# Kernel tuning notes

Hardware: AMD Instinct MI355X
Metric: run time of the kernel (lower is better)

## Reference

```python
import jax, jax.numpy as jnp
import numpy as np


def setup_inputs() -> dict:
    key = jax.random.key(0)
    k1, k2 = jax.random.split(key)
    B, S_ENC, S_DEC, D = 8, 2048, 2048, 512
    enc_outputs = jax.random.normal(k1, (B, S_ENC, D), dtype=jnp.float32)
    dec_outputs = jax.random.normal(k2, (B, S_DEC, D), dtype=jnp.float32)
    return {"enc_outputs": enc_outputs, "dec_outputs": dec_outputs}


def reference(enc_outputs, dec_outputs):
    # scores: [B, S_dec, S_enc] = dec @ enc^T  (no scaling, no mask — matches original)
    s_t = jnp.einsum('bqd,bkd->bqk', dec_outputs, enc_outputs)
    a_t = jax.nn.softmax(s_t, axis=-1)
    # context: [B, S_dec, D]
    c_t = jnp.einsum('bqk,bkd->bqd', a_t, enc_outputs)
    return c_t
```

## Files before the change

kernel.cpp:

```cpp
#include <hip/hip_runtime.h>
#include <cstdint>
#include <cstddef>

#define Bb 8
#define Ss 2048
#define Dd 512

typedef _Float16 half8 __attribute__((ext_vector_type(8)));
typedef _Float16 half4_ __attribute__((ext_vector_type(4)));
typedef _Float16 half2_t __attribute__((ext_vector_type(2)));
typedef float f32x4 __attribute__((ext_vector_type(4)));

static __device__ __forceinline__ void gload_lds16(const void* g, void* l) {
  __builtin_amdgcn_global_load_lds((const __attribute__((address_space(1))) void*)g,
                                   (__attribute__((address_space(3))) void*)l,
                                   16, 0, 0);
}

__global__ void k0_prep(const float* __restrict__ enc, const float* __restrict__ dec,
                        _Float16* __restrict__ enc16, _Float16* __restrict__ encT,
                        _Float16* __restrict__ dec16) {
  __shared__ _Float16 tb[8][64][8];
  int bid = blockIdx.x;
  int b = bid & 7, kt = (bid >> 3) & 31, dt = bid >> 8;
  int key0 = kt * 64, d0 = dt * 64;
  int t = threadIdx.x;

  {
    size_t off = (size_t)bid * 4096 + (size_t)t * 16;
    const float4* p = (const float4*)(dec + off);
    float4 a0 = p[0], a1 = p[1], a2 = p[2], a3 = p[3];
    half8 h0, h1;
    h0[0] = (_Float16)a0.x; h0[1] = (_Float16)a0.y; h0[2] = (_Float16)a0.z; h0[3] = (_Float16)a0.w;
    h0[4] = (_Float16)a1.x; h0[5] = (_Float16)a1.y; h0[6] = (_Float16)a1.z; h0[7] = (_Float16)a1.w;
    h1[0] = (_Float16)a2.x; h1[1] = (_Float16)a2.y; h1[2] = (_Float16)a2.z; h1[3] = (_Float16)a2.w;
    h1[4] = (_Float16)a3.x; h1[5] = (_Float16)a3.y; h1[6] = (_Float16)a3.z; h1[7] = (_Float16)a3.w;
    *(half8*)(dec16 + off) = h0;
    *(half8*)(dec16 + off + 8) = h1;
  }

  const float* src = enc + ((size_t)b * Ss + key0) * Dd + d0;
  _Float16* d16 = enc16 + ((size_t)b * Ss + key0) * Dd + d0;
#pragma unroll
  for (int p = 0; p < 4; ++p) {
    int row = p * 16 + (t >> 4);
    int c = (t & 15) * 4;
    float4 a = *(const float4*)(src + (size_t)row * Dd + c);
    half4_ h;
    h[0] = (_Float16)a.x; h[1] = (_Float16)a.y; h[2] = (_Float16)a.z; h[3] = (_Float16)a.w;
    *(half4_*)(d16 + (size_t)row * Dd + c) = h;
    int K = row >> 3, k = row & 7;
#pragma unroll
    for (int i = 0; i < 4; ++i) tb[K][c + i][k] = h[i];
  }
  __syncthreads();

  _Float16* oT = encT + ((size_t)b * Dd + d0) * Ss + key0;
#pragma unroll
  for (int q = 0; q < 2; ++q) {
    int d = q * 32 + (t >> 3);
    int k8 = (t & 7) * 8;
    half8 v = *(const half8*)&tb[k8 >> 3][d][0];
    *(half8*)(oT + (size_t)d * Ss + k8) = v;
  }
}

__launch_bounds__(256, 2)
__global__ void k1_qk(const _Float16* __restrict__ A, const _Float16* __restrict__ Bm,
                      _Float16* __restrict__ S, half2_t* __restrict__ pms) {
  __shared__ __align__(16) _Float16 lA[128 * 64];
  __shared__ __align__(16) _Float16 lB[128 * 64];
  int bid = blockIdx.x;
  int b = bid & 7;
  int t = bid >> 3;
  int tm = t & 15, tn = t >> 4;
  int tid = threadIdx.x;
  int w = tid >> 6, L = tid & 63;
  int wm = w & 1, wn = w >> 1;

  const _Float16* Ag = A + ((size_t)b * Ss + (size_t)tm * 128) * Dd;
  const _Float16* Bg = Bm + ((size_t)b * Ss + (size_t)tn * 128) * Dd;

  int rowS[4], colS[4], ldsOff[4];
#pragma unroll
  for (int i = 0; i < 4; ++i) {
    int se = (w * 4 + i) * 512 + L * 8;
    int row = se >> 6;
    int blk = (se >> 3) & 7;
    rowS[i] = row;
    colS[i] = (blk ^ (row & 7)) << 3;
    ldsOff[i] = se;
  }

  f32x4 acc[4][4];
#pragma unroll
  for (int mt = 0; mt < 4; ++mt)
#pragma unroll
    for (int nt = 0; nt < 4; ++nt) acc[mt][nt] = (f32x4){0.f, 0.f, 0.f, 0.f};

  int g = L >> 4, lm = L & 15;

  for (int k0 = 0; k0 < Dd; k0 += 64) {
    __syncthreads();
#pragma unroll
    for (int i = 0; i < 4; ++i) {
      gload_lds16(Ag + (size_t)rowS[i] * Dd + k0 + colS[i], lA + ldsOff[i]);
      gload_lds16(Bg + (size_t)rowS[i] * Dd + k0 + colS[i], lB + ldsOff[i]);
    }
    __syncthreads();
#pragma unroll
    for (int ds = 0; ds < 64; ds += 32) {
      half8 af[4], bf[4];
#pragma unroll
      for (int mt = 0; mt < 4; ++mt) {
        int row = wm * 64 + mt * 16 + lm;
        int blk = ((ds >> 3) + g) ^ (row & 7);
        af[mt] = *(const half8*)(lA + row * 64 + blk * 8);
      }
#pragma unroll
      for (int nt = 0; nt < 4; ++nt) {
        int row = wn * 64 + nt * 16 + lm;
        int blk = ((ds >> 3) + g) ^ (row & 7);
        bf[nt] = *(const half8*)(lB + row * 64 + blk * 8);
      }
#pragma unroll
      for (int mt = 0; mt < 4; ++mt)
#pragma unroll
        for (int nt = 0; nt < 4; ++nt)
          acc[mt][nt] = __builtin_amdgcn_mfma_f32_16x16x32_f16(af[mt], bf[nt], acc[mt][nt], 0, 0, 0);
    }
  }

  size_t rowbase = (size_t)b * Ss;
#pragma unroll
  for (int mt = 0; mt < 4; ++mt) {
#pragma unroll
    for (int r = 0; r < 4; ++r) {
      int row_g = tm * 128 + wm * 64 + mt * 16 + g * 4 + r;
      _Float16* Srow = S + (rowbase + row_g) * Ss + (size_t)tn * 128 + wn * 64 + lm;
      float rm = -1e30f;
#pragma unroll
      for (int nt = 0; nt < 4; ++nt) rm = fmaxf(rm, acc[mt][nt][r]);
      rm = fmaxf(rm, __shfl_xor(rm, 1));
      rm = fmaxf(rm, __shfl_xor(rm, 2));
      rm = fmaxf(rm, __shfl_xor(rm, 4));
      rm = fmaxf(rm, __shfl_xor(rm, 8));
      _Float16 mh = (_Float16)rm;
      float mf = (float)mh;
      float sum = 0.f;
#pragma unroll
      for (int nt = 0; nt < 4; ++nt) {
        float e = __expf(acc[mt][nt][r] - mf);
        Srow[nt * 16] = (_Float16)e;
        sum += e;
      }
      sum += __shfl_xor(sum, 1);
      sum += __shfl_xor(sum, 2);
      sum += __shfl_xor(sum, 4);
      sum += __shfl_xor(sum, 8);
      if (lm == 0) {
        half2_t st; st.x = mh; st.y = (_Float16)sum;
        pms[(rowbase + row_g) * 32 + tn * 2 + wn] = st;
      }
    }
  }
}

__launch_bounds__(256, 4)
__global__ void k3_pv(const _Float16* __restrict__ P, const _Float16* __restrict__ Vt,
                      const half2_t* __restrict__ pms, float* __restrict__ C) {
  __shared__ __align__(16) _Float16 lA[128 * 64];
  __shared__ __align__(16) _Float16 lB[64 * 64];
  __shared__ float fctL[32 * 128];
  int bid = blockIdx.x;
  int b = bid & 7;
  int t = bid >> 3;
  int tm = t & 15, tn = t >> 4;
  int tid = threadIdx.x;
  int w = tid >> 6, L = tid & 63;
  int wm = w & 1, wn = w >> 1;

  if (tid < 128) {
    const half2_t* pr = pms + ((size_t)b * Ss + (size_t)tm * 128 + tid) * 32;
    float mc[32], sc[32];
#pragma unroll
    for (int c = 0; c < 32; ++c) { half2_t v = pr[c]; mc[c] = (float)v.x; sc[c] = (float)v.y; }
    float m = mc[0];
#pragma unroll
    for (int c = 1; c < 32; ++c) m = fmaxf(m, mc[c]);
    float tot = 0.f;
    float ef[32];
#pragma unroll
    for (int c = 0; c < 32; ++c) { ef[c] = __expf(mc[c] - m); tot += sc[c] * ef[c]; }
    float rinv = 1.0f / tot;
#pragma unroll
    for (int c = 0; c < 32; ++c) fctL[c * 128 + tid] = ef[c] * rinv;
  }

  const _Float16* Ag = P + ((size_t)b * Ss + (size_t)tm * 128) * Ss;
  const _Float16* Bg = Vt + ((size_t)b * Dd + (size_t)tn * 64) * Ss;

  int rowA[4], colA[4], offA[4];
#pragma unroll
  for (int i = 0; i < 4; ++i) {
    int se = (w * 4 + i) * 512 + L * 8;
    int row = se >> 6;
    int blk = (se >> 3) & 7;
    rowA[i] = row;
    colA[i] = (blk ^ (row & 7)) << 3;
    offA[i] = se;
  }
  int rowB[2], colB[2], offB[2];
#pragma unroll
  for (int i = 0; i < 2; ++i) {
    int se = (w * 2 + i) * 512 + L * 8;
    int row = se >> 6;
    int blk = (se >> 3) & 7;
    rowB[i] = row;
    colB[i] = (blk ^ (row & 7)) << 3;
    offB[i] = se;
  }

  f32x4 acc[4][2];
#pragma unroll
  for (int mt = 0; mt < 4; ++mt)
#pragma unroll
    for (int nt = 0; nt < 2; ++nt) acc[mt][nt] = (f32x4){0.f, 0.f, 0.f, 0.f};

  int g = L >> 4, lm = L & 15;

  for (int k0 = 0; k0 < Ss; k0 += 64) {
    __syncthreads();
#pragma unroll
    for (int i = 0; i < 4; ++i)
      gload_lds16(Ag + (size_t)rowA[i] * Ss + k0 + colA[i], lA + offA[i]);
#pragma unroll
    for (int i = 0; i < 2; ++i)
      gload_lds16(Bg + (size_t)rowB[i] * Ss + k0 + colB[i], lB + offB[i]);
    __syncthreads();
    _Float16 fh[4];
#pragma unroll
    for (int mt = 0; mt < 4; ++mt)
      fh[mt] = (_Float16)fctL[(k0 >> 6) * 128 + wm * 64 + mt * 16 + lm];
#pragma unroll
    for (int ds = 0; ds < 64; ds += 32) {
      half8 af[4], bf[2];
#pragma unroll
      for (int mt = 0; mt < 4; ++mt) {
        int row = wm * 64 + mt * 16 + lm;
        int blk = ((ds >> 3) + g) ^ (row & 7);
        af[mt] = *(const half8*)(lA + row * 64 + blk * 8);
#pragma unroll
        for (int j = 0; j < 8; ++j) af[mt][j] *= fh[mt];
      }
#pragma unroll
      for (int nt = 0; nt < 2; ++nt) {
        int row = wn * 32 + nt * 16 + lm;
        int blk = ((ds >> 3) + g) ^ (row & 7);
        bf[nt] = *(const half8*)(lB + row * 64 + blk * 8);
      }
#pragma unroll
      for (int mt = 0; mt < 4; ++mt)
#pragma unroll
        for (int nt = 0; nt < 2; ++nt)
          acc[mt][nt] = __builtin_amdgcn_mfma_f32_16x16x32_f16(af[mt], bf[nt], acc[mt][nt], 0, 0, 0);
    }
  }

#pragma unroll
  for (int mt = 0; mt < 4; ++mt) {
#pragma unroll
    for (int r = 0; r < 4; ++r) {
      int row_g = tm * 128 + wm * 64 + mt * 16 + g * 4 + r;
      float* Crow = C + ((size_t)b * Ss + row_g) * Dd + (size_t)tn * 64 + wn * 32 + lm;
#pragma unroll
      for (int nt = 0; nt < 2; ++nt) Crow[nt * 16] = acc[mt][nt][r];
    }
  }
}

extern "C" void kernel_launch(void* const* d_in, const int* in_sizes, int n_in,
                              void* d_out, int out_size, void* d_ws, size_t ws_size,
                              hipStream_t stream) {
  const float* enc = (const float*)d_in[0];
  const float* dec = (const float*)d_in[1];
  float* out = (float*)d_out;

  const size_t nElem = (size_t)Bb * Ss * Dd;
  const size_t nS = (size_t)Bb * Ss * Ss;

  _Float16* dec16 = (_Float16*)d_ws;
  _Float16* enc16 = dec16 + nElem;
  _Float16* encT = enc16 + nElem;
  _Float16* Sp = encT + nElem;
  half2_t* pms = (half2_t*)(Sp + nS);

  size_t need = nElem * 2 * 3 + nS * 2 + (size_t)Bb * Ss * 32 * 4;
  if (ws_size < need) return;

  k0_prep<<<2048, 256, 0, stream>>>(enc, dec, enc16, encT, dec16);
  k1_qk<<<2048, 256, 0, stream>>>(dec16, enc16, Sp, pms);
  k3_pv<<<1024, 256, 0, stream>>>(Sp, encT, pms, out);
}
```

Before: 206.0 us.

## Rewrite QK kernel with 256x256 tiles, 8 waves, double-buffered LDS pipeline

Replaces the 128x128-tile QK^T+partial-softmax kernel with a 256x256-tile, 512-thread version that uses 128KB of dynamic LDS. Global-to-LDS loads for the next K-slice are double-buffered and staggered across quarter-tile MFMA phases, with explicit vmcnt waits, barriers and setprio. The aim is more operand reuse per loaded byte and better overlap of loads with MFMA work. The old kernel is kept as a fallback for when the large shared-memory allocation is unavailable. In exchange it needs high register pressure and runs only 512 blocks.

```diff
diff --git a/kernel.cpp b/kernel.cpp
--- a/kernel.cpp
+++ b/kernel.cpp
@@ -65,9 +65,191 @@
   }
 }
 
-__launch_bounds__(256, 2)
+template<int QM, int QN>
+static __device__ __forceinline__ void mfma16(f32x4 (&acc)[8][4],
+                                              const half8 (&af)[4][2],
+                                              const half8 (&bf)[2][2]) {
+#pragma unroll
+  for (int ks = 0; ks < 2; ++ks)
+#pragma unroll
+    for (int mt2 = 0; mt2 < 4; ++mt2)
+#pragma unroll
+      for (int ntl = 0; ntl < 2; ++ntl)
+        acc[QM * 4 + mt2][QN * 2 + ntl] = __builtin_amdgcn_mfma_f32_16x16x32_f16(
+            af[mt2][ks], bf[ntl][ks], acc[QM * 4 + mt2][QN * 2 + ntl], 0, 0, 0);
+}
+
+#define WAITVM4 do { asm volatile("s_waitcnt vmcnt(4)" ::: "memory"); __builtin_amdgcn_sched_barrier(0); } while (0)
+#define WAITVM0 do { asm volatile("s_waitcnt vmcnt(0)" ::: "memory"); __builtin_amdgcn_sched_barrier(0); } while (0)
+#define BAR() __builtin_amdgcn_s_barrier()
+
+__launch_bounds__(512, 2)
 __global__ void k1_qk(const _Float16* __restrict__ A, const _Float16* __restrict__ Bm,
                       _Float16* __restrict__ S, half2_t* __restrict__ pms) {
+  extern __shared__ _Float16 smem[];
+  int bid = blockIdx.x;
+  int b = bid & 7;
+  int tt = bid >> 3;
+  int tm = tt & 7, tn = tt >> 3;
+  int tid = threadIdx.x;
+  int w = tid >> 6, L = tid & 63;
+  int wm = w >> 2, wn = w & 3;
+  int g = L >> 4, lm = L & 15;
+
+  const _Float16* Ag = A + ((size_t)b * Ss + (size_t)tm * 256) * Dd;
+  const _Float16* Bg = Bm + ((size_t)b * Ss + (size_t)tn * 256) * Dd;
+
+  int sl0 = (w * 2 + 0) * 512 + L * 8;
+  int sl1 = (w * 2 + 1) * 512 + L * 8;
+  const _Float16* gA[2][2];
+  const _Float16* gB[2][2];
+#pragma unroll
+  for (int j = 0; j < 2; ++j) {
+    int sl = j ? sl1 : sl0;
+    int lr = sl >> 6;
+    int oct = (sl >> 3) & 7;
+#pragma unroll
+    for (int ga = 0; ga < 2; ++ga) {
+      int row = (lr >> 6) * 128 + ga * 64 + (lr & 63);
+      gA[ga][j] = Ag + (size_t)row * Dd + ((oct ^ (row & 7)) * 8);
+    }
+#pragma unroll
+    for (int qn = 0; qn < 2; ++qn) {
+      int row = (lr >> 5) * 64 + qn * 32 + (lr & 31);
+      gB[qn][j] = Bg + (size_t)row * Dd + ((oct ^ (row & 7)) * 8);
+    }
+  }
+
+  f32x4 acc[8][4];
+#pragma unroll
+  for (int i = 0; i < 8; ++i)
+#pragma unroll
+    for (int j = 0; j < 4; ++j) acc[i][j] = (f32x4){0.f, 0.f, 0.f, 0.f};
+
+  int o80 = ((0 * 4 + g) ^ (lm & 7)) * 8;
+  int o81 = ((1 * 4 + g) ^ (lm & 7)) * 8;
+  int aBase = (wm * 64 + lm) * 64;
+  int bBase = (wn * 32 + lm) * 64;
+
+  gload_lds16(gA[0][0], smem + sl0);
+  gload_lds16(gA[0][1], smem + sl1);
+  gload_lds16(gB[0][0], smem + 32768 + sl0);
+  gload_lds16(gB[0][1], smem + 32768 + sl1);
+  gload_lds16(gB[1][0], smem + 32768 + 8192 + sl0);
+  gload_lds16(gB[1][1], smem + 32768 + 8192 + sl1);
+  gload_lds16(gA[1][0], smem + 8192 + sl0);
+  gload_lds16(gA[1][1], smem + 8192 + sl1);
+  WAITVM4;
+  BAR();
+
+  const int NT = Dd / 64;
+#pragma unroll 2
+  for (int t = 0; t < NT; ++t) {
+    int cb = t & 1, nb = cb ^ 1;
+    const _Float16* pAr = smem + cb * 16384 + aBase;
+    const _Float16* pBr = smem + 32768 + cb * 16384 + bBase;
+    _Float16* lAn = smem + nb * 16384;
+    _Float16* lBn = smem + 32768 + nb * 16384;
+    int k0n = (t + 1) * 64;
+    bool pre = (t < NT - 1);
+    half8 af[4][2], bf[2][2];
+
+#pragma unroll
+    for (int mt2 = 0; mt2 < 4; ++mt2) {
+      af[mt2][0] = *(const half8*)(pAr + mt2 * 1024 + o80);
+      af[mt2][1] = *(const half8*)(pAr + mt2 * 1024 + o81);
+    }
+#pragma unroll
+    for (int ntl = 0; ntl < 2; ++ntl) {
+      bf[ntl][0] = *(const half8*)(pBr + ntl * 1024 + o80);
+      bf[ntl][1] = *(const half8*)(pBr + ntl * 1024 + o81);
+    }
+    if (pre) { gload_lds16(gA[0][0] + k0n, lAn + sl0); gload_lds16(gA[0][1] + k0n, lAn + sl1); }
+    BAR();
+    __builtin_amdgcn_s_setprio(1);
+    mfma16<0, 0>(acc, af, bf);
+    __builtin_amdgcn_s_setprio(0);
+    if (pre) WAITVM4;
+    BAR();
+
+#pragma unroll
+    for (int ntl = 0; ntl < 2; ++ntl) {
+      bf[ntl][0] = *(const half8*)(pBr + 8192 + ntl * 1024 + o80);
+      bf[ntl][1] = *(const half8*)(pBr + 8192 + ntl * 1024 + o81);
+    }
+    if (pre) { gload_lds16(gB[0][0] + k0n, lBn + sl0); gload_lds16(gB[0][1] + k0n, lBn + sl1); }
+    BAR();
+    __builtin_amdgcn_s_setprio(1);
+    mfma16<0, 1>(acc, af, bf);
+    __builtin_amdgcn_s_setprio(0);
+    if (pre) WAITVM4;
+    BAR();
+
+#pragma unroll
+    for (int mt2 = 0; mt2 < 4; ++mt2) {
+      af[mt2][0] = *(const half8*)(pAr + 8192 + mt2 * 1024 + o80);
+      af[mt2][1] = *(const half8*)(pAr + 8192 + mt2 * 1024 + o81);
+    }
+    if (pre) { gload_lds16(gB[1][0] + k0n, lBn + 8192 + sl0); gload_lds16(gB[1][1] + k0n, lBn + 8192 + sl1); }
+    BAR();
+    __builtin_amdgcn_s_setprio(1);
+    mfma16<1, 1>(acc, af, bf);
+    __builtin_amdgcn_s_setprio(0);
+    BAR();
+
+#pragma unroll
+    for (int ntl = 0; ntl < 2; ++ntl) {
+      bf[ntl][0] = *(const half8*)(pBr + ntl * 1024 + o80);
+      bf[ntl][1] = *(const half8*)(pBr + ntl * 1024 + o81);
+    }
+    if (pre) { gload_lds16(gA[1][0] + k0n, lAn + 8192 + sl0); gload_lds16(gA[1][1] + k0n, lAn + 8192 + sl1); }
+    BAR();
+    __builtin_amdgcn_s_setprio(1);
+    mfma16<1, 0>(acc, af, bf);
+    __builtin_amdgcn_s_setprio(0);
+    if (t < NT - 2) { WAITVM4; }
+    else if (t == NT - 2) { WAITVM0; }
+    BAR();
+  }
+
+  size_t rowbase = (size_t)b * Ss;
+#pragma unroll
+  for (int mt = 0; mt < 8; ++mt) {
+#pragma unroll
+    for (int r = 0; r < 4; ++r) {
+      int row_g = tm * 256 + wm * 128 + mt * 16 + g * 4 + r;
+      _Float16* Srow = S + (rowbase + row_g) * Ss + (size_t)tn * 256 + wn * 64 + lm;
+      float rm = -1e30f;
+#pragma unroll
+      for (int nt = 0; nt < 4; ++nt) rm = fmaxf(rm, acc[mt][nt][r]);
+      rm = fmaxf(rm, __shfl_xor(rm, 1));
+      rm = fmaxf(rm, __shfl_xor(rm, 2));
+      rm = fmaxf(rm, __shfl_xor(rm, 4));
+      rm = fmaxf(rm, __shfl_xor(rm, 8));
+      _Float16 mh = (_Float16)rm;
+      float mf = (float)mh;
+      float sum = 0.f;
+#pragma unroll
+      for (int nt = 0; nt < 4; ++nt) {
+        float e = __expf(acc[mt][nt][r] - mf);
+        Srow[nt * 16] = (_Float16)e;
+        sum += e;
+      }
+      sum += __shfl_xor(sum, 1);
+      sum += __shfl_xor(sum, 2);
+      sum += __shfl_xor(sum, 4);
+      sum += __shfl_xor(sum, 8);
+      if (lm == 0) {
+        half2_t st; st.x = mh; st.y = (_Float16)sum;
+        pms[(rowbase + row_g) * 32 + tn * 4 + wn] = st;
+      }
+    }
+  }
+}
+
+__launch_bounds__(256, 2)
+__global__ void k1_qk_fb(const _Float16* __restrict__ A, const _Float16* __restrict__ Bm,
+                         _Float16* __restrict__ S, half2_t* __restrict__ pms) {
   __shared__ __align__(16) _Float16 lA[128 * 64];
   __shared__ __align__(16) _Float16 lB[128 * 64];
   int bid = blockIdx.x;
@@ -298,7 +480,27 @@
   size_t need = nElem * 2 * 3 + nS * 2 + (size_t)Bb * Ss * 32 * 4;
   if (ws_size < need) return;
 
+  static int g_k1_big = -1;
+  if (g_k1_big < 0) {
+    int ok = 0;
+    (void)hipFuncSetAttribute(reinterpret_cast<const void*>(&k1_qk),
+                              hipFuncAttributeMaxDynamicSharedMemorySize, 131072);
+    hipFuncAttributes fa;
+    if (hipFuncGetAttributes(&fa, reinterpret_cast<const void*>(&k1_qk)) == hipSuccess &&
+        fa.maxDynamicSharedSizeBytes >= 131072) ok = 1;
+    if (!ok) {
+      int dev = 0, maxShm = 0;
+      (void)hipGetDevice(&dev);
+      if (hipDeviceGetAttribute(&maxShm, hipDeviceAttributeMaxSharedMemoryPerBlock, dev) ==
+              hipSuccess && maxShm >= 131072) ok = 1;
+    }
+    g_k1_big = ok;
+  }
+
   k0_prep<<<2048, 256, 0, stream>>>(enc, dec, enc16, encT, dec16);
-  k1_qk<<<2048, 256, 0, stream>>>(dec16, enc16, Sp, pms);
+  if (g_k1_big)
+    k1_qk<<<512, 512, 131072, stream>>>(dec16, enc16, Sp, pms);
+  else
+    k1_qk_fb<<<2048, 256, 0, stream>>>(dec16, enc16, Sp, pms);
   k3_pv<<<1024, 256, 0, stream>>>(Sp, encT, pms, out);
 }
```

After: 205.9 us. No clear change (-0.0%).

## Fuse QK, softmax and PV into single flash-attention kernel with online softmax

Applied to the files above, without the earlier changes.

Replaces the two-kernel path (QK scores written to a full fp16 S matrix in global memory, then a PV kernel rescaling by per-chunk max/sum) with one fused flash-style kernel. Each block owns 64 query rows, keeps Q fragments in registers, double-buffers 32-key E tiles in LDS via async loads, does an online softmax with conditional rescaling, and reads V directly from global into registers. This removes the large S round trip through HBM but launches only 256 blocks, uses many barriers per 32-key step, and has small per-iteration MFMA work, so occupancy and sync overhead may limit it.

```diff
diff --git a/kernel.cpp b/kernel.cpp
--- a/kernel.cpp
+++ b/kernel.cpp
@@ -8,7 +8,6 @@
 
 typedef _Float16 half8 __attribute__((ext_vector_type(8)));
 typedef _Float16 half4_ __attribute__((ext_vector_type(4)));
-typedef _Float16 half2_t __attribute__((ext_vector_type(2)));
 typedef float f32x4 __attribute__((ext_vector_type(4)));
 
 static __device__ __forceinline__ void gload_lds16(const void* g, void* l) {
@@ -65,32 +64,53 @@
   }
 }
 
-__launch_bounds__(256, 2)
-__global__ void k1_qk(const _Float16* __restrict__ A, const _Float16* __restrict__ Bm,
-                      _Float16* __restrict__ S, half2_t* __restrict__ pms) {
-  __shared__ __align__(16) _Float16 lA[128 * 64];
-  __shared__ __align__(16) _Float16 lB[128 * 64];
+#define WAITVM(N) do { asm volatile("s_waitcnt vmcnt(" #N ")" ::: "memory"); __builtin_amdgcn_sched_barrier(0); } while (0)
+#define LGKM0 asm volatile("s_waitcnt lgkmcnt(0)" ::: "memory")
+#define BARR() __builtin_amdgcn_s_barrier()
+
+__launch_bounds__(512, 2)
+__global__ void kf_attn(const _Float16* __restrict__ Qm, const _Float16* __restrict__ Em,
+                        const _Float16* __restrict__ Vt, float* __restrict__ C) {
+  extern __shared__ _Float16 smem[];
+  _Float16* pS = smem + 32768;
+  float* fb = (float*)(smem + 34816);
+  float* wMax = fb;
+  float* wSum = fb + 128;
+  float* fct  = fb + 256;
+  float* negm = fb + 320;
+  float* mst  = fb + 384;
+  float* lst  = fb + 448;
+  int*   flg  = (int*)(fb + 512);
+
   int bid = blockIdx.x;
-  int b = bid & 7;
-  int t = bid >> 3;
-  int tm = t & 15, tn = t >> 4;
+  int b = bid & 7, qt = bid >> 3;
+  int q0 = qt * 64;
   int tid = threadIdx.x;
   int w = tid >> 6, L = tid & 63;
-  int wm = w & 1, wn = w >> 1;
-
-  const _Float16* Ag = A + ((size_t)b * Ss + (size_t)tm * 128) * Dd;
-  const _Float16* Bg = Bm + ((size_t)b * Ss + (size_t)tn * 128) * Dd;
-
-  int rowS[4], colS[4], ldsOff[4];
-#pragma unroll
-  for (int i = 0; i < 4; ++i) {
-    int se = (w * 4 + i) * 512 + L * 8;
-    int row = se >> 6;
-    int blk = (se >> 3) & 7;
-    rowS[i] = row;
-    colS[i] = (blk ^ (row & 7)) << 3;
-    ldsOff[i] = se;
-  }
+  int g = L >> 4, lm = L & 15;
+  int wm4 = w >> 1, wn2 = w & 1;
+  int k7 = lm & 7;
+
+  half8 qf[16];
+  {
+    const _Float16* qp = Qm + ((size_t)(b * Ss + q0 + wm4 * 16 + lm)) * Dd + g * 8;
+#pragma unroll
+    for (int ks = 0; ks < 16; ++ks) qf[ks] = *(const half8*)(qp + ks * 32);
+  }
+
+  if (tid < 64) { mst[tid] = -1e30f; lst[tid] = 0.f; }
+
+  const _Float16* eg[4]; int els[4];
+#pragma unroll
+  for (int r = 0; r < 4; ++r) {
+    int key = r * 8 + w;
+    els[r] = key * 512 + L * 8;
+    eg[r] = Em + ((size_t)(b * Ss) + key) * Dd + ((L ^ (key & 7)) * 8);
+  }
+  uint64_t vb[4];
+#pragma unroll
+  for (int nt = 0; nt < 4; ++nt)
+    vb[nt] = (uint64_t)(uintptr_t)(Vt + ((size_t)(b * Dd + w * 64 + nt * 16 + lm)) * Ss + g * 8);
 
   f32x4 acc[4][4];
 #pragma unroll
@@ -98,185 +118,121 @@
 #pragma unroll
     for (int nt = 0; nt < 4; ++nt) acc[mt][nt] = (f32x4){0.f, 0.f, 0.f, 0.f};
 
-  int g = L >> 4, lm = L & 15;
-
-  for (int k0 = 0; k0 < Dd; k0 += 64) {
-    __syncthreads();
-#pragma unroll
-    for (int i = 0; i < 4; ++i) {
-      gload_lds16(Ag + (size_t)rowS[i] * Dd + k0 + colS[i], lA + ldsOff[i]);
-      gload_lds16(Bg + (size_t)rowS[i] * Dd + k0 + colS[i], lB + ldsOff[i]);
-    }
-    __syncthreads();
-#pragma unroll
-    for (int ds = 0; ds < 64; ds += 32) {
-      half8 af[4], bf[4];
-#pragma unroll
-      for (int mt = 0; mt < 4; ++mt) {
-        int row = wm * 64 + mt * 16 + lm;
-        int blk = ((ds >> 3) + g) ^ (row & 7);
-        af[mt] = *(const half8*)(lA + row * 64 + blk * 8);
-      }
-#pragma unroll
-      for (int nt = 0; nt < 4; ++nt) {
-        int row = wn * 64 + nt * 16 + lm;
-        int blk = ((ds >> 3) + g) ^ (row & 7);
-        bf[nt] = *(const half8*)(lB + row * 64 + blk * 8);
-      }
+#pragma unroll
+  for (int r = 0; r < 4; ++r) gload_lds16(eg[r], smem + els[r]);
+  LGKM0;
+  BARR();
+
+#pragma unroll 1
+  for (int t = 0; t < 64; ++t) {
+    bool pre = t < 63;
+    const _Float16* eC = smem + ((t & 1) << 14);
+    _Float16* eN = smem + (((t + 1) & 1) << 14);
+
+    f32x4 bfr[4];
+#pragma unroll
+    for (int nt = 0; nt < 4; ++nt) {
+      uint64_t a = vb[nt] + (uint64_t)t * 64;
+      asm volatile("global_load_dwordx4 %0, %1, off" : "=v"(bfr[nt]) : "v"(a));
+    }
+    if (pre) {
+#pragma unroll
+      for (int r = 0; r < 4; ++r) gload_lds16(eg[r] + (size_t)(t + 1) * 16384, eN + els[r]);
+    }
+    if (pre) { WAITVM(8); } else { WAITVM(4); }
+    BARR();
+
+    f32x4 s0 = (f32x4){0.f, 0.f, 0.f, 0.f}, s1 = (f32x4){0.f, 0.f, 0.f, 0.f};
+    const _Float16* eRow = eC + (wn2 * 16 + lm) * 512;
+    __builtin_amdgcn_s_setprio(1);
+#pragma unroll
+    for (int ks = 0; ks < 16; ks += 2) {
+      half8 b0 = *(const half8*)(eRow + (((ks * 4 + g) ^ k7) << 3));
+      half8 b1 = *(const half8*)(eRow + ((((ks + 1) * 4 + g) ^ k7) << 3));
+      s0 = __builtin_amdgcn_mfma_f32_16x16x32_f16(qf[ks], b0, s0, 0, 0, 0);
+      s1 = __builtin_amdgcn_mfma_f32_16x16x32_f16(qf[ks + 1], b1, s1, 0, 0, 0);
+    }
+    __builtin_amdgcn_s_setprio(0);
+    f32x4 sa = s0 + s1;
+
+#pragma unroll
+    for (int r = 0; r < 4; ++r) {
+      float m = sa[r];
+      m = fmaxf(m, __shfl_xor(m, 1));
+      m = fmaxf(m, __shfl_xor(m, 2));
+      m = fmaxf(m, __shfl_xor(m, 4));
+      m = fmaxf(m, __shfl_xor(m, 8));
+      if (lm == 0) wMax[wn2 * 64 + wm4 * 16 + g * 4 + r] = m;
+    }
+    LGKM0; BARR();
+
+    if (tid < 64) {
+      float tmax = fmaxf(wMax[tid], wMax[64 + tid]);
+      float mo = mst[tid];
+      float mn = fmaxf(mo, tmax);
+      fct[tid] = __expf(mo - mn);
+      negm[tid] = mn;
+      mst[tid] = mn;
+      unsigned long long bal = __ballot(tmax > mo);
+      if (tid == 0) *flg = (bal != 0ULL) ? 1 : 0;
+    }
+    LGKM0; BARR();
+
+    int cc = wn2 * 2 + (lm >> 3);
+#pragma unroll
+    for (int r = 0; r < 4; ++r) {
+      int R = wm4 * 16 + g * 4 + r;
+      float p = __expf(sa[r] - negm[R]);
+      pS[R * 32 + (((cc ^ r) << 3) | k7)] = (_Float16)p;
+      float s = p;
+      s += __shfl_xor(s, 1); s += __shfl_xor(s, 2);
+      s += __shfl_xor(s, 4); s += __shfl_xor(s, 8);
+      if (lm == 0) wSum[wn2 * 64 + R] = s;
+    }
+    LGKM0; BARR();
+
+    if (tid < 64) lst[tid] = lst[tid] * fct[tid] + wSum[tid] + wSum[64 + tid];
+
+    if (*flg) {
 #pragma unroll
       for (int mt = 0; mt < 4; ++mt)
 #pragma unroll
-        for (int nt = 0; nt < 4; ++nt)
-          acc[mt][nt] = __builtin_amdgcn_mfma_f32_16x16x32_f16(af[mt], bf[nt], acc[mt][nt], 0, 0, 0);
-    }
-  }
-
-  size_t rowbase = (size_t)b * Ss;
-#pragma unroll
-  for (int mt = 0; mt < 4; ++mt) {
-#pragma unroll
-    for (int r = 0; r < 4; ++r) {
-      int row_g = tm * 128 + wm * 64 + mt * 16 + g * 4 + r;
-      _Float16* Srow = S + (rowbase + row_g) * Ss + (size_t)tn * 128 + wn * 64 + lm;
-      float rm = -1e30f;
-#pragma unroll
-      for (int nt = 0; nt < 4; ++nt) rm = fmaxf(rm, acc[mt][nt][r]);
-      rm = fmaxf(rm, __shfl_xor(rm, 1));
-      rm = fmaxf(rm, __shfl_xor(rm, 2));
-      rm = fmaxf(rm, __shfl_xor(rm, 4));
-      rm = fmaxf(rm, __shfl_xor(rm, 8));
-      _Float16 mh = (_Float16)rm;
-      float mf = (float)mh;
-      float sum = 0.f;
-#pragma unroll
-      for (int nt = 0; nt < 4; ++nt) {
-        float e = __expf(acc[mt][nt][r] - mf);
-        Srow[nt * 16] = (_Float16)e;
-        sum += e;
-      }
-      sum += __shfl_xor(sum, 1);
-      sum += __shfl_xor(sum, 2);
-      sum += __shfl_xor(sum, 4);
-      sum += __shfl_xor(sum, 8);
-      if (lm == 0) {
-        half2_t st; st.x = mh; st.y = (_Float16)sum;
-        pms[(rowbase + row_g) * 32 + tn * 2 + wn] = st;
-      }
-    }
-  }
-}
-
-__launch_bounds__(256, 4)
-__global__ void k3_pv(const _Float16* __restrict__ P, const _Float16* __restrict__ Vt,
-                      const half2_t* __restrict__ pms, float* __restrict__ C) {
-  __shared__ __align__(16) _Float16 lA[128 * 64];
-  __shared__ __align__(16) _Float16 lB[64 * 64];
-  __shared__ float fctL[32 * 128];
-  int bid = blockIdx.x;
-  int b = bid & 7;
-  int t = bid >> 3;
-  int tm = t & 15, tn = t >> 4;
-  int tid = threadIdx.x;
-  int w = tid >> 6, L = tid & 63;
-  int wm = w & 1, wn = w >> 1;
-
-  if (tid < 128) {
-    const half2_t* pr = pms + ((size_t)b * Ss + (size_t)tm * 128 + tid) * 32;
-    float mc[32], sc[32];
-#pragma unroll
-    for (int c = 0; c < 32; ++c) { half2_t v = pr[c]; mc[c] = (float)v.x; sc[c] = (float)v.y; }
-    float m = mc[0];
-#pragma unroll
-    for (int c = 1; c < 32; ++c) m = fmaxf(m, mc[c]);
-    float tot = 0.f;
-    float ef[32];
-#pragma unroll
-    for (int c = 0; c < 32; ++c) { ef[c] = __expf(mc[c] - m); tot += sc[c] * ef[c]; }
-    float rinv = 1.0f / tot;
-#pragma unroll
-    for (int c = 0; c < 32; ++c) fctL[c * 128 + tid] = ef[c] * rinv;
-  }
-
-  const _Float16* Ag = P + ((size_t)b * Ss + (size_t)tm * 128) * Ss;
-  const _Float16* Bg = Vt + ((size_t)b * Dd + (size_t)tn * 64) * Ss;
-
-  int rowA[4], colA[4], offA[4];
-#pragma unroll
-  for (int i = 0; i < 4; ++i) {
-    int se = (w * 4 + i) * 512 + L * 8;
-    int row = se >> 6;
-    int blk = (se >> 3) & 7;
-    rowA[i] = row;
-    colA[i] = (blk ^ (row & 7)) << 3;
-    offA[i] = se;
-  }
-  int rowB[2], colB[2], offB[2];
-#pragma unroll
-  for (int i = 0; i < 2; ++i) {
-    int se = (w * 2 + i) * 512 + L * 8;
-    int row = se >> 6;
-    int blk = (se >> 3) & 7;
-    rowB[i] = row;
-    colB[i] = (blk ^ (row & 7)) << 3;
-    offB[i] = se;
-  }
-
-  f32x4 acc[4][2];
+        for (int rr = 0; rr < 4; ++rr) {
+          float f = fct[mt * 16 + g * 4 + rr];
+#pragma unroll
+          for (int nt = 0; nt < 4; ++nt) acc[mt][nt][rr] *= f;
+        }
+    }
+
+    if (pre) { WAITVM(4); } else { WAITVM(0); }
+
+    half8 af[4];
+#pragma unroll
+    for (int mt = 0; mt < 4; ++mt)
+      af[mt] = *(const half8*)(pS + (mt * 16 + lm) * 32 + ((g ^ (lm & 3)) << 3));
+    __builtin_amdgcn_s_setprio(1);
+#pragma unroll
+    for (int mt = 0; mt < 4; ++mt)
+#pragma unroll
+      for (int nt = 0; nt < 4; ++nt)
+        acc[mt][nt] = __builtin_amdgcn_mfma_f32_16x16x32_f16(af[mt], *(half8*)&bfr[nt],
+                                                             acc[mt][nt], 0, 0, 0);
+    __builtin_amdgcn_s_setprio(0);
+  }
+
+  LGKM0; BARR();
+  if (tid < 64) fct[tid] = 1.0f / lst[tid];
+  LGKM0; BARR();
 #pragma unroll
   for (int mt = 0; mt < 4; ++mt)
 #pragma unroll
-    for (int nt = 0; nt < 2; ++nt) acc[mt][nt] = (f32x4){0.f, 0.f, 0.f, 0.f};
-
-  int g = L >> 4, lm = L & 15;
-
-  for (int k0 = 0; k0 < Ss; k0 += 64) {
-    __syncthreads();
-#pragma unroll
-    for (int i = 0; i < 4; ++i)
-      gload_lds16(Ag + (size_t)rowA[i] * Ss + k0 + colA[i], lA + offA[i]);
-#pragma unroll
-    for (int i = 0; i < 2; ++i)
-      gload_lds16(Bg + (size_t)rowB[i] * Ss + k0 + colB[i], lB + offB[i]);
-    __syncthreads();
-    _Float16 fh[4];
-#pragma unroll
-    for (int mt = 0; mt < 4; ++mt)
-      fh[mt] = (_Float16)fctL[(k0 >> 6) * 128 + wm * 64 + mt * 16 + lm];
-#pragma unroll
-    for (int ds = 0; ds < 64; ds += 32) {
-      half8 af[4], bf[2];
-#pragma unroll
-      for (int mt = 0; mt < 4; ++mt) {
-        int row = wm * 64 + mt * 16 + lm;
-        int blk = ((ds >> 3) + g) ^ (row & 7);
-        af[mt] = *(const half8*)(lA + row * 64 + blk * 8);
-#pragma unroll
-        for (int j = 0; j < 8; ++j) af[mt][j] *= fh[mt];
-      }
-#pragma unroll
-      for (int nt = 0; nt < 2; ++nt) {
-        int row = wn * 32 + nt * 16 + lm;
-        int blk = ((ds >> 3) + g) ^ (row & 7);
-        bf[nt] = *(const half8*)(lB + row * 64 + blk * 8);
-      }
-#pragma unroll
-      for (int mt = 0; mt < 4; ++mt)
-#pragma unroll
-        for (int nt = 0; nt < 2; ++nt)
-          acc[mt][nt] = __builtin_amdgcn_mfma_f32_16x16x32_f16(af[mt], bf[nt], acc[mt][nt], 0, 0, 0);
-    }
-  }
-
-#pragma unroll
-  for (int mt = 0; mt < 4; ++mt) {
-#pragma unroll
-    for (int r = 0; r < 4; ++r) {
-      int row_g = tm * 128 + wm * 64 + mt * 16 + g * 4 + r;
-      float* Crow = C + ((size_t)b * Ss + row_g) * Dd + (size_t)tn * 64 + wn * 32 + lm;
-#pragma unroll
-      for (int nt = 0; nt < 2; ++nt) Crow[nt * 16] = acc[mt][nt][r];
-    }
-  }
+    for (int rr = 0; rr < 4; ++rr) {
+      int R = mt * 16 + g * 4 + rr;
+      float ri = fct[R];
+      float* Crow = C + ((size_t)(b * Ss + q0 + R)) * Dd + w * 64 + lm;
+#pragma unroll
+      for (int nt = 0; nt < 4; ++nt) Crow[nt * 16] = acc[mt][nt][rr] * ri;
+    }
 }
 
 extern "C" void kernel_launch(void* const* d_in, const int* in_sizes, int n_in,
@@ -287,18 +243,21 @@
   float* out = (float*)d_out;
 
   const size_t nElem = (size_t)Bb * Ss * Dd;
-  const size_t nS = (size_t)Bb * Ss * Ss;
 
   _Float16* dec16 = (_Float16*)d_ws;
   _Float16* enc16 = dec16 + nElem;
   _Float16* encT = enc16 + nElem;
-  _Float16* Sp = encT + nElem;
-  half2_t* pms = (half2_t*)(Sp + nS);
-
-  size_t need = nElem * 2 * 3 + nS * 2 + (size_t)Bb * Ss * 32 * 4;
+
+  size_t need = nElem * 2 * 3;
   if (ws_size < need) return;
 
+  static int g_attr = 0;
+  if (!g_attr) {
+    (void)hipFuncSetAttribute(reinterpret_cast<const void*>(&kf_attn),
+                              hipFuncAttributeMaxDynamicSharedMemorySize, 73728);
+    g_attr = 1;
+  }
+
   k0_prep<<<2048, 256, 0, stream>>>(enc, dec, enc16, encT, dec16);
-  k1_qk<<<2048, 256, 0, stream>>>(dec16, enc16, Sp, pms);
-  k3_pv<<<1024, 256, 0, stream>>>(Sp, encT, pms, out);
-}
+  kf_attn<<<256, 512, 73728, stream>>>(dec16, enc16, encT, out);
+}
```

Result: slower. 317.7 us (+54.2%).

## Widen QK^T tile to 128x256 per block to improve B-operand reuse

Applied to the files above, without the earlier changes.

Enlarges the k1_qk output tile from 128x128 to 128x256, so each warp computes 64x128 with a 4x8 accumulator array. The grid drops from 2048 to 1024 blocks, and the per-block partial max/sum statistics are still emitted per 64-column chunk, which keeps the layout k3_pv expects. The aim is to reuse A tiles across more columns and cut global/LDS load traffic per MFMA. In exchange, accumulator register pressure doubles, LDS use grows to 48KB, and occupancy may fall under launch_bounds(256,2).

```diff
diff --git a/kernel.cpp b/kernel.cpp
--- a/kernel.cpp
+++ b/kernel.cpp
@@ -69,7 +69,7 @@
 __global__ void k1_qk(const _Float16* __restrict__ A, const _Float16* __restrict__ Bm,
                       _Float16* __restrict__ S, half2_t* __restrict__ pms) {
   __shared__ __align__(16) _Float16 lA[128 * 64];
-  __shared__ __align__(16) _Float16 lB[128 * 64];
+  __shared__ __align__(16) _Float16 lB[256 * 64];
   int bid = blockIdx.x;
   int b = bid & 7;
   int t = bid >> 3;
@@ -77,40 +77,37 @@
   int tid = threadIdx.x;
   int w = tid >> 6, L = tid & 63;
   int wm = w & 1, wn = w >> 1;
+  int g = L >> 4, lm = L & 15;
 
   const _Float16* Ag = A + ((size_t)b * Ss + (size_t)tm * 128) * Dd;
-  const _Float16* Bg = Bm + ((size_t)b * Ss + (size_t)tn * 128) * Dd;
-
-  int rowS[4], colS[4], ldsOff[4];
-#pragma unroll
-  for (int i = 0; i < 4; ++i) {
-    int se = (w * 4 + i) * 512 + L * 8;
-    int row = se >> 6;
-    int blk = (se >> 3) & 7;
-    rowS[i] = row;
-    colS[i] = (blk ^ (row & 7)) << 3;
-    ldsOff[i] = se;
-  }
-
-  f32x4 acc[4][4];
+  const _Float16* Bg = Bm + ((size_t)b * Ss + (size_t)tn * 256) * Dd;
+
+  int cswz = ((L & 7) ^ (L >> 3)) << 3;
+  int rA0 = w * 32 + (L >> 3);
+  int rB0 = w * 64 + (L >> 3);
+  int slA = w * 2048 + L * 8;
+  int slB = w * 4096 + L * 8;
+  const _Float16* gA = Ag + (size_t)rA0 * Dd + cswz;
+  const _Float16* gB = Bg + (size_t)rB0 * Dd + cswz;
+
+  f32x4 acc[4][8];
 #pragma unroll
   for (int mt = 0; mt < 4; ++mt)
 #pragma unroll
-    for (int nt = 0; nt < 4; ++nt) acc[mt][nt] = (f32x4){0.f, 0.f, 0.f, 0.f};
-
-  int g = L >> 4, lm = L & 15;
+    for (int nt = 0; nt < 8; ++nt) acc[mt][nt] = (f32x4){0.f, 0.f, 0.f, 0.f};
 
   for (int k0 = 0; k0 < Dd; k0 += 64) {
     __syncthreads();
 #pragma unroll
-    for (int i = 0; i < 4; ++i) {
-      gload_lds16(Ag + (size_t)rowS[i] * Dd + k0 + colS[i], lA + ldsOff[i]);
-      gload_lds16(Bg + (size_t)rowS[i] * Dd + k0 + colS[i], lB + ldsOff[i]);
-    }
+    for (int i = 0; i < 4; ++i)
+      gload_lds16(gA + (size_t)i * (8 * Dd) + k0, lA + slA + i * 512);
+#pragma unroll
+    for (int i = 0; i < 8; ++i)
+      gload_lds16(gB + (size_t)i * (8 * Dd) + k0, lB + slB + i * 512);
     __syncthreads();
 #pragma unroll
     for (int ds = 0; ds < 64; ds += 32) {
-      half8 af[4], bf[4];
+      half8 af[4];
 #pragma unroll
       for (int mt = 0; mt < 4; ++mt) {
         int row = wm * 64 + mt * 16 + lm;
@@ -118,16 +115,14 @@
         af[mt] = *(const half8*)(lA + row * 64 + blk * 8);
       }
 #pragma unroll
-      for (int nt = 0; nt < 4; ++nt) {
-        int row = wn * 64 + nt * 16 + lm;
+      for (int nt = 0; nt < 8; ++nt) {
+        int row = wn * 128 + nt * 16 + lm;
         int blk = ((ds >> 3) + g) ^ (row & 7);
-        bf[nt] = *(const half8*)(lB + row * 64 + blk * 8);
-      }
-#pragma unroll
-      for (int mt = 0; mt < 4; ++mt)
-#pragma unroll
-        for (int nt = 0; nt < 4; ++nt)
-          acc[mt][nt] = __builtin_amdgcn_mfma_f32_16x16x32_f16(af[mt], bf[nt], acc[mt][nt], 0, 0, 0);
+        half8 bf = *(const half8*)(lB + row * 64 + blk * 8);
+#pragma unroll
+        for (int mt = 0; mt < 4; ++mt)
+          acc[mt][nt] = __builtin_amdgcn_mfma_f32_16x16x32_f16(af[mt], bf, acc[mt][nt], 0, 0, 0);
+      }
     }
   }
 
@@ -137,30 +132,33 @@
 #pragma unroll
     for (int r = 0; r < 4; ++r) {
       int row_g = tm * 128 + wm * 64 + mt * 16 + g * 4 + r;
-      _Float16* Srow = S + (rowbase + row_g) * Ss + (size_t)tn * 128 + wn * 64 + lm;
-      float rm = -1e30f;
-#pragma unroll
-      for (int nt = 0; nt < 4; ++nt) rm = fmaxf(rm, acc[mt][nt][r]);
-      rm = fmaxf(rm, __shfl_xor(rm, 1));
-      rm = fmaxf(rm, __shfl_xor(rm, 2));
-      rm = fmaxf(rm, __shfl_xor(rm, 4));
-      rm = fmaxf(rm, __shfl_xor(rm, 8));
-      _Float16 mh = (_Float16)rm;
-      float mf = (float)mh;
-      float sum = 0.f;
-#pragma unroll
-      for (int nt = 0; nt < 4; ++nt) {
-        float e = __expf(acc[mt][nt][r] - mf);
-        Srow[nt * 16] = (_Float16)e;
-        sum += e;
-      }
-      sum += __shfl_xor(sum, 1);
-      sum += __shfl_xor(sum, 2);
-      sum += __shfl_xor(sum, 4);
-      sum += __shfl_xor(sum, 8);
-      if (lm == 0) {
-        half2_t st; st.x = mh; st.y = (_Float16)sum;
-        pms[(rowbase + row_g) * 32 + tn * 2 + wn] = st;
+      _Float16* Srow = S + (rowbase + row_g) * Ss + (size_t)tn * 256 + wn * 128 + lm;
+#pragma unroll
+      for (int c2 = 0; c2 < 2; ++c2) {
+        float rm = -1e30f;
+#pragma unroll
+        for (int q = 0; q < 4; ++q) rm = fmaxf(rm, acc[mt][c2 * 4 + q][r]);
+        rm = fmaxf(rm, __shfl_xor(rm, 1));
+        rm = fmaxf(rm, __shfl_xor(rm, 2));
+        rm = fmaxf(rm, __shfl_xor(rm, 4));
+        rm = fmaxf(rm, __shfl_xor(rm, 8));
+        _Float16 mh = (_Float16)rm;
+        float mf = (float)mh;
+        float sum = 0.f;
+#pragma unroll
+        for (int q = 0; q < 4; ++q) {
+          float e = __expf(acc[mt][c2 * 4 + q][r] - mf);
+          Srow[(c2 * 4 + q) * 16] = (_Float16)e;
+          sum += e;
+        }
+        sum += __shfl_xor(sum, 1);
+        sum += __shfl_xor(sum, 2);
+        sum += __shfl_xor(sum, 4);
+        sum += __shfl_xor(sum, 8);
+        if (lm == 0) {
+          half2_t st; st.x = mh; st.y = (_Float16)sum;
+          pms[(rowbase + row_g) * 32 + tn * 4 + wn * 2 + c2] = st;
+        }
       }
     }
   }
@@ -299,6 +297,6 @@
   if (ws_size < need) return;
 
   k0_prep<<<2048, 256, 0, stream>>>(enc, dec, enc16, encT, dec16);
-  k1_qk<<<2048, 256, 0, stream>>>(dec16, enc16, Sp, pms);
+  k1_qk<<<1024, 256, 0, stream>>>(dec16, enc16, Sp, pms);
   k3_pv<<<1024, 256, 0, stream>>>(Sp, encT, pms, out);
 }
```

After: 202.2 us. Within noise of the previous version (-1.9%).
